# Performance work log

Measured on AMD Instinct MI355X. Metric: run time of the kernel, lower is better.

The kernel has to match this reference:

```python
import jax, jax.numpy as jnp
import numpy as np

L, B, S, D = 12, 2, 2048, 768
QK, H, V = 128, 512, 32000
SCALE = 128 ** (-0.5)


def setup_inputs() -> dict:
    key = jax.random.key(0)
    ks = jax.random.split(key, 11)
    p = lambda k, shp: jax.random.normal(k, shp, dtype=jnp.float32) * 0.02
    return {
        "layer_outputs": jax.random.normal(ks[0], (L, B, S, D), dtype=jnp.float32),
        "Wq": p(ks[1], (D, QK)), "bq": jnp.zeros((QK,), jnp.float32),
        "Wk": p(ks[2], (D, QK)), "bk": jnp.zeros((QK,), jnp.float32),
        "Wv": p(ks[3], (D, H)),  "bv": jnp.zeros((H,), jnp.float32),
        "W1": p(ks[4], (H, H // 2)), "b1": jnp.zeros((H // 2,), jnp.float32),
        "W2": p(ks[5], (H // 2, V)), "b2": jnp.zeros((V,), jnp.float32),
    }


def reference(layer_outputs, Wq, bq, Wk, bk, Wv, bv, W1, b1, W2, b2):
    # layer_outputs: (L, B, S, D) -> h: (S, L, B, D) as in torch permute(2,0,1,3)
    h = jnp.transpose(layer_outputs, (2, 0, 1, 3))
    q_in = h.mean(axis=1)                              # (S, B, D)
    q = jax.nn.relu(q_in @ Wq + bq)                    # (S, B, 128)
    k = jax.nn.relu(h @ Wk + bk)                       # (S, L, B, 128)
    scores = jnp.einsum('sbd,slbd->slb', q, k)[..., None] * SCALE  # (S, L, B, 1)
    attn = jax.nn.softmax(scores, axis=1)              # softmax over layer axis
    v = h @ Wv + bv                                    # (S, L, B, H)
    agg = jnp.sum(attn * v, axis=1)                    # (S, B, H)
    agg = jnp.transpose(agg, (1, 0, 2))                # (B, S, H)
    mid = jax.nn.relu(agg @ W1 + b1)                   # (B, S, H//2); dropout is eval-mode identity
    return mid @ W2 + b2                               # (B, S, V)
```

## Files before the change

kernel.cpp:

```cpp
#include <hip/hip_runtime.h>

#define Snum 2048
#define SCALE 0.08838834764831845f

typedef __attribute__((ext_vector_type(8))) __bf16 bf16x8;
typedef __attribute__((ext_vector_type(4))) float f32x4;

__device__ inline unsigned short f2bf(float f) {
    unsigned int u = __float_as_uint(f);
    unsigned int r = u + 0x7FFFu + ((u >> 16) & 1u);
    return (unsigned short)(r >> 16);
}
__device__ inline float bf2f(unsigned short u) {
    return __uint_as_float(((unsigned)u) << 16);
}
__device__ inline void gld_lds16(const unsigned short* g, unsigned short* l) {
    __builtin_amdgcn_global_load_lds(
        (const __attribute__((address_space(1))) unsigned int*)g,
        (__attribute__((address_space(3))) unsigned int*)l, 16, 0, 0);
}

__global__ __launch_bounds__(256) void transpose_f2bf(
    const float* __restrict__ in, unsigned short* __restrict__ out, int K, int N)
{
    __shared__ float t[32][33];
    const int bx = blockIdx.x;
    const int by = blockIdx.y;
    const int tx = threadIdx.x & 31, ty = threadIdx.x >> 5;
    #pragma unroll
    for (int i = 0; i < 4; ++i) {
        int k = by * 32 + ty + i * 8, n = bx * 32 + tx;
        t[ty + i * 8][tx] = in[(size_t)k * N + n];
    }
    __syncthreads();
    #pragma unroll
    for (int i = 0; i < 4; ++i) {
        int n = bx * 32 + ty + i * 8, k = by * 32 + tx;
        out[(size_t)n * K + k] = f2bf(t[tx][ty + i * 8]);
    }
}

__global__ __launch_bounds__(256) void mean_kernel(
    const float* __restrict__ x, unsigned short* __restrict__ hmean)
{
    int idx = blockIdx.x * 256 + threadIdx.x;
    if (idx >= 4096 * 192) return;
    int r = idx / 192, jv = idx % 192;
    int b = r >> 11, s = r & 2047;
    float a0 = 0.f, a1 = 0.f, a2 = 0.f, a3 = 0.f;
    #pragma unroll
    for (int l = 0; l < 12; ++l) {
        const float4 v = *(const float4*)(x + ((size_t)(l * 2 + b) * Snum + s) * 768 + jv * 4);
        a0 += v.x; a1 += v.y; a2 += v.z; a3 += v.w;
    }
    const float inv = 1.0f / 12.0f;
    ushort4 o;
    o.x = f2bf(a0 * inv); o.y = f2bf(a1 * inv); o.z = f2bf(a2 * inv); o.w = f2bf(a3 * inv);
    *(ushort4*)(hmean + (size_t)r * 768 + jv * 4) = o;
}

__global__ __launch_bounds__(256) void scores_hbar(
    const float* __restrict__ x,
    const unsigned short* __restrict__ Q,
    const unsigned short* __restrict__ Kall,
    unsigned short* __restrict__ hbar)
{
    const int wid = threadIdx.x >> 6, lane = threadIdx.x & 63;
    const int r = blockIdx.x * 4 + wid;
    const int b = r >> 11, s = r & 2047;

    const unsigned short* qrow = Q + (size_t)r * 128 + lane * 2;
    const float q0 = bf2f(qrow[0]), q1 = bf2f(qrow[1]);

    float sc[12];
    #pragma unroll
    for (int l = 0; l < 12; ++l) {
        const unsigned short* krow = Kall + ((size_t)(l * 2 + b) * Snum + s) * 128 + lane * 2;
        float p = q0 * bf2f(krow[0]) + q1 * bf2f(krow[1]);
        #pragma unroll
        for (int off = 32; off > 0; off >>= 1) p += __shfl_xor(p, off, 64);
        sc[l] = p * SCALE;
    }
    float m = sc[0];
    #pragma unroll
    for (int l = 1; l < 12; ++l) m = fmaxf(m, sc[l]);
    float att[12], den = 0.f;
    #pragma unroll
    for (int l = 0; l < 12; ++l) { att[l] = __expf(sc[l] - m); den += att[l]; }
    const float inv = 1.0f / den;
    #pragma unroll
    for (int l = 0; l < 12; ++l) att[l] *= inv;

    #pragma unroll
    for (int jv = 0; jv < 3; ++jv) {
        const int d0 = jv * 256 + lane * 4;
        float a0 = 0.f, a1 = 0.f, a2 = 0.f, a3 = 0.f;
        #pragma unroll
        for (int l = 0; l < 12; ++l) {
            const float4 v = *(const float4*)(x + ((size_t)(l * 2 + b) * Snum + s) * 768 + d0);
            a0 += att[l] * v.x; a1 += att[l] * v.y; a2 += att[l] * v.z; a3 += att[l] * v.w;
        }
        ushort4 o;
        o.x = f2bf(a0); o.y = f2bf(a1); o.z = f2bf(a2); o.w = f2bf(a3);
        *(ushort4*)(hbar + (size_t)r * 768 + d0) = o;
    }
}

template <int RELU, int OUT_BF16>
__global__ __launch_bounds__(256) void gemm64(
    const unsigned short* __restrict__ A, const unsigned short* __restrict__ Bt,
    const float* __restrict__ bias, void* __restrict__ out, int M, int N, int K)
{
    __shared__ __align__(16) unsigned short As[64][40];
    __shared__ __align__(16) unsigned short Bs[64][40];
    const int tid = threadIdx.x;
    const int bn = blockIdx.x, bm = blockIdx.y;
    const int wid = tid >> 6, lane = tid & 63;
    const int wm = (wid >> 1) * 32, wn = (wid & 1) * 32;
    const int lr = lane & 15, g = lane >> 4;
    const int r0 = bm * 64, c0 = bn * 64;

    f32x4 acc[2][2] = {};
    const int row = tid >> 2, kc = (tid & 3) * 8;

    for (int k0 = 0; k0 < K; k0 += 32) {
        __syncthreads();
        *(uint4*)&As[row][kc] = *(const uint4*)(A  + (size_t)(r0 + row) * K + k0 + kc);
        *(uint4*)&Bs[row][kc] = *(const uint4*)(Bt + (size_t)(c0 + row) * K + k0 + kc);
        __syncthreads();

        bf16x8 aF[2], bF[2];
        #pragma unroll
        for (int mm = 0; mm < 2; ++mm) aF[mm] = *(const bf16x8*)&As[wm + mm * 16 + lr][g * 8];
        #pragma unroll
        for (int nn = 0; nn < 2; ++nn) bF[nn] = *(const bf16x8*)&Bs[wn + nn * 16 + lr][g * 8];
        #pragma unroll
        for (int mm = 0; mm < 2; ++mm)
            #pragma unroll
            for (int nn = 0; nn < 2; ++nn)
                acc[mm][nn] = __builtin_amdgcn_mfma_f32_16x16x32_bf16(aF[mm], bF[nn], acc[mm][nn], 0, 0, 0);
    }

    #pragma unroll
    for (int mm = 0; mm < 2; ++mm)
        #pragma unroll
        for (int nn = 0; nn < 2; ++nn) {
            int col = c0 + wn + nn * 16 + lr;
            float bcol = bias[col];
            #pragma unroll
            for (int reg = 0; reg < 4; ++reg) {
                int orow = r0 + wm + mm * 16 + g * 4 + reg;
                float v = acc[mm][nn][reg] + bcol;
                if (RELU) v = v > 0.f ? v : 0.f;
                if (OUT_BF16) ((unsigned short*)out)[(size_t)orow * N + col] = f2bf(v);
                else          ((float*)out)[(size_t)orow * N + col] = v;
            }
        }
}

template <int AF32, int RELU, int OUT_BF16>
__global__ __launch_bounds__(256) void gemm128(
    const void* __restrict__ Ap, const unsigned short* __restrict__ Bt,
    const float* __restrict__ bias, void* __restrict__ out, int M, int N, int K)
{
    __shared__ __align__(16) unsigned short As[128 * 32];
    __shared__ __align__(16) unsigned short Bs[128 * 32];
    const int tid = threadIdx.x;
    const int bn = blockIdx.x, bm = blockIdx.y;
    const int wid = tid >> 6, lane = tid & 63;
    const int wm = (wid >> 1) * 64, wn = (wid & 1) * 64;
    const int lr = lane & 15, g = lane >> 4;
    const int r0 = bm * 128, c0 = bn * 128;

    f32x4 acc[4][4] = {};

    for (int k0 = 0; k0 < K; k0 += 32) {
        __syncthreads();
        if (AF32) {
            const float* Af = (const float*)Ap;
            const int arow = tid >> 1, akc = (tid & 1) * 16;
            const float* src = Af + (size_t)(r0 + arow) * K + k0 + akc;
            unsigned short v[16];
            #pragma unroll
            for (int j = 0; j < 16; ++j) v[j] = f2bf(src[j]);
            *(uint4*)&As[arow * 32 + akc]     = *(uint4*)&v[0];
            *(uint4*)&As[arow * 32 + akc + 8] = *(uint4*)&v[8];
        } else {
            const unsigned short* Ab = (const unsigned short*)Ap;
            #pragma unroll
            for (int c = 0; c < 2; ++c) {
                int rr = wid * 32 + c * 16;
                gld_lds16(Ab + (size_t)(r0 + rr + (lane >> 2)) * K + k0 + (lane & 3) * 8,
                          &As[rr * 32]);
            }
        }
        #pragma unroll
        for (int c = 0; c < 2; ++c) {
            int rr = wid * 32 + c * 16;
            gld_lds16(Bt + (size_t)(c0 + rr + (lane >> 2)) * K + k0 + (lane & 3) * 8,
                      &Bs[rr * 32]);
        }
        __syncthreads();

        bf16x8 aF[4], bF[4];
        #pragma unroll
        for (int mm = 0; mm < 4; ++mm) aF[mm] = *(const bf16x8*)&As[(wm + mm * 16 + lr) * 32 + g * 8];
        #pragma unroll
        for (int nn = 0; nn < 4; ++nn) bF[nn] = *(const bf16x8*)&Bs[(wn + nn * 16 + lr) * 32 + g * 8];
        #pragma unroll
        for (int mm = 0; mm < 4; ++mm)
            #pragma unroll
            for (int nn = 0; nn < 4; ++nn)
                acc[mm][nn] = __builtin_amdgcn_mfma_f32_16x16x32_bf16(aF[mm], bF[nn], acc[mm][nn], 0, 0, 0);
    }

    #pragma unroll
    for (int mm = 0; mm < 4; ++mm)
        #pragma unroll
        for (int nn = 0; nn < 4; ++nn) {
            int col = c0 + wn + nn * 16 + lr;
            float bcol = bias[col];
            #pragma unroll
            for (int reg = 0; reg < 4; ++reg) {
                int orow = r0 + wm + mm * 16 + g * 4 + reg;
                float v = acc[mm][nn][reg] + bcol;
                if (RELU) v = v > 0.f ? v : 0.f;
                if (OUT_BF16) ((unsigned short*)out)[(size_t)orow * N + col] = f2bf(v);
                else          ((float*)out)[(size_t)orow * N + col] = v;
            }
        }
}

extern "C" void kernel_launch(void* const* d_in, const int* in_sizes, int n_in,
                              void* d_out, int out_size, void* d_ws, size_t ws_size,
                              hipStream_t stream) {
    (void)in_sizes; (void)n_in; (void)out_size; (void)ws_size;

    const float* x  = (const float*)d_in[0];
    const float* Wq = (const float*)d_in[1];
    const float* bq = (const float*)d_in[2];
    const float* Wk = (const float*)d_in[3];
    const float* bk = (const float*)d_in[4];
    const float* Wv = (const float*)d_in[5];
    const float* bv = (const float*)d_in[6];
    const float* W1 = (const float*)d_in[7];
    const float* b1 = (const float*)d_in[8];
    const float* W2 = (const float*)d_in[9];
    const float* b2 = (const float*)d_in[10];

    char* p = (char*)d_ws;
    unsigned short* Wqt   = (unsigned short*)p; p += (size_t)128 * 768 * 2;
    unsigned short* Wkt   = (unsigned short*)p; p += (size_t)128 * 768 * 2;
    unsigned short* Wvt   = (unsigned short*)p; p += (size_t)512 * 768 * 2;
    unsigned short* W1t   = (unsigned short*)p; p += (size_t)256 * 512 * 2;
    unsigned short* W2t   = (unsigned short*)p; p += (size_t)32000 * 256 * 2;
    unsigned short* hmean = (unsigned short*)p; p += (size_t)4096 * 768 * 2;
    unsigned short* Qb    = (unsigned short*)p; p += (size_t)4096 * 128 * 2;
    unsigned short* Kall  = (unsigned short*)p; p += (size_t)49152 * 128 * 2;
    unsigned short* hbar  = (unsigned short*)p; p += (size_t)4096 * 768 * 2;
    unsigned short* aggb  = (unsigned short*)p; p += (size_t)4096 * 512 * 2;
    unsigned short* midb  = (unsigned short*)p; p += (size_t)4096 * 256 * 2;

    transpose_f2bf<<<dim3(128 / 32, 768 / 32), dim3(256), 0, stream>>>(Wq, Wqt, 768, 128);
    transpose_f2bf<<<dim3(128 / 32, 768 / 32), dim3(256), 0, stream>>>(Wk, Wkt, 768, 128);
    transpose_f2bf<<<dim3(512 / 32, 768 / 32), dim3(256), 0, stream>>>(Wv, Wvt, 768, 512);
    transpose_f2bf<<<dim3(256 / 32, 512 / 32), dim3(256), 0, stream>>>(W1, W1t, 512, 256);
    transpose_f2bf<<<dim3(32000 / 32, 256 / 32), dim3(256), 0, stream>>>(W2, W2t, 256, 32000);

    mean_kernel<<<dim3(3072), dim3(256), 0, stream>>>(x, hmean);

    gemm64<1, 1><<<dim3(128 / 64, 4096 / 64), dim3(256), 0, stream>>>(
        hmean, Wqt, bq, Qb, 4096, 128, 768);

    gemm128<1, 1, 1><<<dim3(128 / 128, 49152 / 128), dim3(256), 0, stream>>>(
        x, Wkt, bk, Kall, 49152, 128, 768);

    scores_hbar<<<dim3(1024), dim3(256), 0, stream>>>(x, Qb, Kall, hbar);

    gemm128<0, 0, 1><<<dim3(512 / 128, 4096 / 128), dim3(256), 0, stream>>>(
        hbar, Wvt, bv, aggb, 4096, 512, 768);

    gemm64<1, 1><<<dim3(256 / 64, 4096 / 64), dim3(256), 0, stream>>>(
        aggb, W1t, b1, midb, 4096, 256, 512);

    gemm128<0, 0, 0><<<dim3(32000 / 128, 4096 / 128), dim3(256), 0, stream>>>(
        midb, W2t, b2, d_out, 4096, 32000, 256);
}
```

Measured before the change: 349.0 us.

## Fuse Q and K projections by projecting per-layer then averaging, swizzle output GEMM

Since the mean over layers is linear, Q is computed by projecting every layer with Wq alongside Wk in one fused 256-wide GEMM over x, then averaging the projections in a small reduction kernel. This removes the separate mean pass and the second read of the large fp32 input, at the cost of extra MFMA work and writing and reading an intermediate per-layer Q buffer. The final vocabulary GEMM gets a specialized kernel with a block-index swizzle so concurrently running blocks share weight tiles in cache. The value GEMM switches to 64-wide tiles for more blocks.

```diff
diff --git a/kernel.cpp b/kernel.cpp
--- a/kernel.cpp
+++ b/kernel.cpp
@@ -40,23 +40,99 @@
     }
 }
 
-__global__ __launch_bounds__(256) void mean_kernel(
-    const float* __restrict__ x, unsigned short* __restrict__ hmean)
-{
-    int idx = blockIdx.x * 256 + threadIdx.x;
-    if (idx >= 4096 * 192) return;
-    int r = idx / 192, jv = idx % 192;
-    int b = r >> 11, s = r & 2047;
-    float a0 = 0.f, a1 = 0.f, a2 = 0.f, a3 = 0.f;
+__global__ __launch_bounds__(512) void proj_qk(
+    const float* __restrict__ x, const unsigned short* __restrict__ Bt,
+    const float* __restrict__ bk,
+    unsigned short* __restrict__ Kall,
+    unsigned short* __restrict__ Pq)
+{
+    __shared__ __align__(16) unsigned short As[128 * 32];
+    __shared__ __align__(16) unsigned short Bs[256 * 32];
+    const int tid = threadIdx.x;
+    const int wid = tid >> 6, lane = tid & 63;
+    const int wm = (wid >> 2) * 64, wn = (wid & 3) * 64;
+    const int lr = lane & 15, g = lane >> 4;
+    const int r0 = blockIdx.x * 128;
+    const int K = 768;
+
+    f32x4 acc[4][4] = {};
+    const int arow = tid >> 2, akc = (tid & 2) * 4;
+    const int arow2 = tid >> 2, akc2 = (tid & 3) * 8;
+    (void)arow; (void)akc;
+
+    for (int k0 = 0; k0 < K; k0 += 32) {
+        __syncthreads();
+        {
+            const float* src = x + (size_t)(r0 + arow2) * K + k0 + akc2;
+            float4 v0 = *(const float4*)src;
+            float4 v1 = *(const float4*)(src + 4);
+            unsigned short v[8];
+            v[0] = f2bf(v0.x); v[1] = f2bf(v0.y); v[2] = f2bf(v0.z); v[3] = f2bf(v0.w);
+            v[4] = f2bf(v1.x); v[5] = f2bf(v1.y); v[6] = f2bf(v1.z); v[7] = f2bf(v1.w);
+            *(uint4*)&As[arow2 * 32 + akc2] = *(uint4*)v;
+        }
+        #pragma unroll
+        for (int c = 0; c < 2; ++c) {
+            int rr = wid * 32 + c * 16;
+            gld_lds16(Bt + (size_t)(rr + (lane >> 2)) * K + k0 + (lane & 3) * 8,
+                      &Bs[rr * 32]);
+        }
+        __syncthreads();
+
+        bf16x8 aF[4], bF[4];
+        #pragma unroll
+        for (int mm = 0; mm < 4; ++mm) aF[mm] = *(const bf16x8*)&As[(wm + mm * 16 + lr) * 32 + g * 8];
+        #pragma unroll
+        for (int nn = 0; nn < 4; ++nn) bF[nn] = *(const bf16x8*)&Bs[(wn + nn * 16 + lr) * 32 + g * 8];
+        #pragma unroll
+        for (int mm = 0; mm < 4; ++mm)
+            #pragma unroll
+            for (int nn = 0; nn < 4; ++nn)
+                acc[mm][nn] = __builtin_amdgcn_mfma_f32_16x16x32_bf16(aF[mm], bF[nn], acc[mm][nn], 0, 0, 0);
+    }
+
+    #pragma unroll
+    for (int mm = 0; mm < 4; ++mm)
+        #pragma unroll
+        for (int nn = 0; nn < 4; ++nn) {
+            int col = wn + nn * 16 + lr;
+            #pragma unroll
+            for (int reg = 0; reg < 4; ++reg) {
+                int orow = r0 + wm + mm * 16 + g * 4 + reg;
+                float v = acc[mm][nn][reg];
+                if (col < 128) {
+                    float kv = v + bk[col];
+                    Kall[(size_t)orow * 128 + col] = f2bf(kv > 0.f ? kv : 0.f);
+                } else {
+                    Pq[(size_t)orow * 128 + (col - 128)] = f2bf(v);
+                }
+            }
+        }
+}
+
+__global__ __launch_bounds__(256) void qreduce(
+    const unsigned short* __restrict__ Pq, const float* __restrict__ bq,
+    unsigned short* __restrict__ Q)
+{
+    const int t = blockIdx.x * 256 + threadIdx.x;
+    const int r = t >> 4, jg = t & 15;
+    const int b = r >> 11, s = r & 2047;
+    float acc[8] = {};
     #pragma unroll
     for (int l = 0; l < 12; ++l) {
-        const float4 v = *(const float4*)(x + ((size_t)(l * 2 + b) * Snum + s) * 768 + jv * 4);
-        a0 += v.x; a1 += v.y; a2 += v.z; a3 += v.w;
-    }
-    const float inv = 1.0f / 12.0f;
-    ushort4 o;
-    o.x = f2bf(a0 * inv); o.y = f2bf(a1 * inv); o.z = f2bf(a2 * inv); o.w = f2bf(a3 * inv);
-    *(ushort4*)(hmean + (size_t)r * 768 + jv * 4) = o;
+        const unsigned short* src = Pq + ((size_t)(l * 2 + b) * Snum + s) * 128 + jg * 8;
+        uint4 u = *(const uint4*)src;
+        const unsigned short* v = (const unsigned short*)&u;
+        #pragma unroll
+        for (int i = 0; i < 8; ++i) acc[i] += bf2f(v[i]);
+    }
+    unsigned short o[8];
+    #pragma unroll
+    for (int i = 0; i < 8; ++i) {
+        float q = acc[i] * (1.0f / 12.0f) + bq[jg * 8 + i];
+        o[i] = f2bf(q > 0.f ? q : 0.f);
+    }
+    *(uint4*)(Q + (size_t)r * 128 + jg * 8) = *(uint4*)o;
 }
 
 __global__ __launch_bounds__(256) void scores_hbar(
@@ -158,15 +234,19 @@
         }
 }
 
-template <int AF32, int RELU, int OUT_BF16>
-__global__ __launch_bounds__(256) void gemm128(
-    const void* __restrict__ Ap, const unsigned short* __restrict__ Bt,
-    const float* __restrict__ bias, void* __restrict__ out, int M, int N, int K)
+__global__ __launch_bounds__(256) void gemm_out(
+    const unsigned short* __restrict__ A,
+    const unsigned short* __restrict__ Bt,
+    const float* __restrict__ bias, float* __restrict__ out)
 {
     __shared__ __align__(16) unsigned short As[128 * 32];
     __shared__ __align__(16) unsigned short Bs[128 * 32];
+    const int K = 256, N = 32000;
+    const int orig = blockIdx.x;
+    const int swz = (orig & 7) * 1000 + (orig >> 3);
+    const int bn = swz >> 5;
+    const int bm = swz & 31;
     const int tid = threadIdx.x;
-    const int bn = blockIdx.x, bm = blockIdx.y;
     const int wid = tid >> 6, lane = tid & 63;
     const int wm = (wid >> 1) * 64, wn = (wid & 1) * 64;
     const int lr = lane & 15, g = lane >> 4;
@@ -176,29 +256,11 @@
 
     for (int k0 = 0; k0 < K; k0 += 32) {
         __syncthreads();
-        if (AF32) {
-            const float* Af = (const float*)Ap;
-            const int arow = tid >> 1, akc = (tid & 1) * 16;
-            const float* src = Af + (size_t)(r0 + arow) * K + k0 + akc;
-            unsigned short v[16];
-            #pragma unroll
-            for (int j = 0; j < 16; ++j) v[j] = f2bf(src[j]);
-            *(uint4*)&As[arow * 32 + akc]     = *(uint4*)&v[0];
-            *(uint4*)&As[arow * 32 + akc + 8] = *(uint4*)&v[8];
-        } else {
-            const unsigned short* Ab = (const unsigned short*)Ap;
-            #pragma unroll
-            for (int c = 0; c < 2; ++c) {
-                int rr = wid * 32 + c * 16;
-                gld_lds16(Ab + (size_t)(r0 + rr + (lane >> 2)) * K + k0 + (lane & 3) * 8,
-                          &As[rr * 32]);
-            }
-        }
         #pragma unroll
         for (int c = 0; c < 2; ++c) {
             int rr = wid * 32 + c * 16;
-            gld_lds16(Bt + (size_t)(c0 + rr + (lane >> 2)) * K + k0 + (lane & 3) * 8,
-                      &Bs[rr * 32]);
+            gld_lds16(A  + (size_t)(r0 + rr + (lane >> 2)) * K + k0 + (lane & 3) * 8, &As[rr * 32]);
+            gld_lds16(Bt + (size_t)(c0 + rr + (lane >> 2)) * K + k0 + (lane & 3) * 8, &Bs[rr * 32]);
         }
         __syncthreads();
 
@@ -223,10 +285,7 @@
             #pragma unroll
             for (int reg = 0; reg < 4; ++reg) {
                 int orow = r0 + wm + mm * 16 + g * 4 + reg;
-                float v = acc[mm][nn][reg] + bcol;
-                if (RELU) v = v > 0.f ? v : 0.f;
-                if (OUT_BF16) ((unsigned short*)out)[(size_t)orow * N + col] = f2bf(v);
-                else          ((float*)out)[(size_t)orow * N + col] = v;
+                out[(size_t)orow * N + col] = acc[mm][nn][reg] + bcol;
             }
         }
 }
@@ -249,40 +308,34 @@
     const float* b2 = (const float*)d_in[10];
 
     char* p = (char*)d_ws;
-    unsigned short* Wqt   = (unsigned short*)p; p += (size_t)128 * 768 * 2;
-    unsigned short* Wkt   = (unsigned short*)p; p += (size_t)128 * 768 * 2;
+    unsigned short* Wqkt  = (unsigned short*)p; p += (size_t)256 * 768 * 2;
     unsigned short* Wvt   = (unsigned short*)p; p += (size_t)512 * 768 * 2;
     unsigned short* W1t   = (unsigned short*)p; p += (size_t)256 * 512 * 2;
     unsigned short* W2t   = (unsigned short*)p; p += (size_t)32000 * 256 * 2;
-    unsigned short* hmean = (unsigned short*)p; p += (size_t)4096 * 768 * 2;
     unsigned short* Qb    = (unsigned short*)p; p += (size_t)4096 * 128 * 2;
     unsigned short* Kall  = (unsigned short*)p; p += (size_t)49152 * 128 * 2;
+    unsigned short* Pq    = (unsigned short*)p; p += (size_t)49152 * 128 * 2;
     unsigned short* hbar  = (unsigned short*)p; p += (size_t)4096 * 768 * 2;
     unsigned short* aggb  = (unsigned short*)p; p += (size_t)4096 * 512 * 2;
     unsigned short* midb  = (unsigned short*)p; p += (size_t)4096 * 256 * 2;
 
-    transpose_f2bf<<<dim3(128 / 32, 768 / 32), dim3(256), 0, stream>>>(Wq, Wqt, 768, 128);
-    transpose_f2bf<<<dim3(128 / 32, 768 / 32), dim3(256), 0, stream>>>(Wk, Wkt, 768, 128);
+    transpose_f2bf<<<dim3(128 / 32, 768 / 32), dim3(256), 0, stream>>>(Wk, Wqkt, 768, 128);
+    transpose_f2bf<<<dim3(128 / 32, 768 / 32), dim3(256), 0, stream>>>(Wq, Wqkt + (size_t)128 * 768, 768, 128);
     transpose_f2bf<<<dim3(512 / 32, 768 / 32), dim3(256), 0, stream>>>(Wv, Wvt, 768, 512);
     transpose_f2bf<<<dim3(256 / 32, 512 / 32), dim3(256), 0, stream>>>(W1, W1t, 512, 256);
     transpose_f2bf<<<dim3(32000 / 32, 256 / 32), dim3(256), 0, stream>>>(W2, W2t, 256, 32000);
 
-    mean_kernel<<<dim3(3072), dim3(256), 0, stream>>>(x, hmean);
-
-    gemm64<1, 1><<<dim3(128 / 64, 4096 / 64), dim3(256), 0, stream>>>(
-        hmean, Wqt, bq, Qb, 4096, 128, 768);
-
-    gemm128<1, 1, 1><<<dim3(128 / 128, 49152 / 128), dim3(256), 0, stream>>>(
-        x, Wkt, bk, Kall, 49152, 128, 768);
+    proj_qk<<<dim3(49152 / 128), dim3(512), 0, stream>>>(x, Wqkt, bk, Kall, Pq);
+
+    qreduce<<<dim3(4096 * 16 / 256), dim3(256), 0, stream>>>(Pq, bq, Qb);
 
     scores_hbar<<<dim3(1024), dim3(256), 0, stream>>>(x, Qb, Kall, hbar);
 
-    gemm128<0, 0, 1><<<dim3(512 / 128, 4096 / 128), dim3(256), 0, stream>>>(
+    gemm64<0, 1><<<dim3(512 / 64, 4096 / 64), dim3(256), 0, stream>>>(
         hbar, Wvt, bv, aggb, 4096, 512, 768);
 
     gemm64<1, 1><<<dim3(256 / 64, 4096 / 64), dim3(256), 0, stream>>>(
         aggb, W1t, b1, midb, 4096, 256, 512);
 
-    gemm128<0, 0, 0><<<dim3(32000 / 128, 4096 / 128), dim3(256), 0, stream>>>(
-        midb, W2t, b2, d_out, 4096, 32000, 256);
-}
+    gemm_out<<<dim3(8000), dim3(256), 0, stream>>>(midb, W2t, b2, (float*)d_out);
+}
```

Result: faster. 340.8 us (-2.3%).
